# Kernel tuning notes

Hardware: AMD Instinct MI355X
Metric: run time of the kernel (lower is better)

Reference implementation:

```python
import jax, jax.numpy as jnp
import numpy as np

N_NODES = 100000
N_EDGES = 6400000
DIM_FEAT = 5


def setup_inputs() -> dict:
    key = jax.random.key(0)
    k1, k2, k3 = jax.random.split(key, 3)
    features = jax.random.normal(k1, (N_NODES, DIM_FEAT), dtype=jnp.float32)
    src = jax.random.randint(k2, (N_EDGES,), 0, N_NODES, dtype=jnp.int64)
    dst = jax.random.randint(k3, (N_EDGES,), 0, N_NODES, dtype=jnp.int64)
    return {"features": features, "src": src, "dst": dst}


def reference(features, src, dst):
    # copy_u('h','m') then sum('m','h'):
    # h_out[v] = sum over edges (u->v) of features[u]
    msgs = features[src]  # [E, F] gather
    h = jax.ops.segment_sum(msgs, dst, num_segments=N_NODES)  # [N, F]
    return h
```

## Files before the change

kernel.cpp:

```cpp
#include <hip/hip_runtime.h>
#include <hip/hip_bf16.h>


#define NN     100000
#define FD     5
#define NOUTT  (NN * FD)
#define NPS    32
#define NPS_SH 5
#define NB     3125
#define NSB    512
#define BLK    256

typedef int vint4 __attribute__((ext_vector_type(4)));

__device__ inline unsigned bf16rtn(float x) {
    unsigned u = __float_as_uint(x);
    u += 0x7fffu + ((u >> 16) & 1u);
    return u >> 16;
}
__device__ inline float lo16(unsigned v) { return __uint_as_float(v << 16); }
__device__ inline float hi16(unsigned v) { return __uint_as_float(v & 0xffff0000u); }

__global__ __launch_bounds__(BLK) void k2_hist(const int* __restrict__ dst,
                                               unsigned short* __restrict__ bh,
                                               int chunk) {
    __shared__ int h[NB];
    for (int b = threadIdx.x; b < NB; b += BLK) h[b] = 0;
    __syncthreads();
    long long e0 = (long long)blockIdx.x * chunk;
    const vint4* d4 = (const vint4*)(dst + e0);
    int n4 = chunk >> 2;
    int i = threadIdx.x;
    for (; i + 3 * BLK < n4; i += 4 * BLK) {
        vint4 d0 = __builtin_nontemporal_load(&d4[i]);
        vint4 d1 = __builtin_nontemporal_load(&d4[i + BLK]);
        vint4 d2 = __builtin_nontemporal_load(&d4[i + 2 * BLK]);
        vint4 d3 = __builtin_nontemporal_load(&d4[i + 3 * BLK]);
        __builtin_amdgcn_sched_barrier(0);
        atomicAdd(&h[d0[0] >> NPS_SH], 1); atomicAdd(&h[d0[1] >> NPS_SH], 1);
        atomicAdd(&h[d0[2] >> NPS_SH], 1); atomicAdd(&h[d0[3] >> NPS_SH], 1);
        atomicAdd(&h[d1[0] >> NPS_SH], 1); atomicAdd(&h[d1[1] >> NPS_SH], 1);
        atomicAdd(&h[d1[2] >> NPS_SH], 1); atomicAdd(&h[d1[3] >> NPS_SH], 1);
        atomicAdd(&h[d2[0] >> NPS_SH], 1); atomicAdd(&h[d2[1] >> NPS_SH], 1);
        atomicAdd(&h[d2[2] >> NPS_SH], 1); atomicAdd(&h[d2[3] >> NPS_SH], 1);
        atomicAdd(&h[d3[0] >> NPS_SH], 1); atomicAdd(&h[d3[1] >> NPS_SH], 1);
        atomicAdd(&h[d3[2] >> NPS_SH], 1); atomicAdd(&h[d3[3] >> NPS_SH], 1);
    }
    for (; i < n4; i += BLK) {
        vint4 d = __builtin_nontemporal_load(&d4[i]);
        atomicAdd(&h[d[0] >> NPS_SH], 1); atomicAdd(&h[d[1] >> NPS_SH], 1);
        atomicAdd(&h[d[2] >> NPS_SH], 1); atomicAdd(&h[d[3] >> NPS_SH], 1);
    }
    __syncthreads();
    unsigned short* row = bh + (size_t)blockIdx.x * NB;
    for (int b = threadIdx.x; b < NB; b += BLK) row[b] = (unsigned short)h[b];
}

__global__ __launch_bounds__(BLK) void k3_scanblk(unsigned short* __restrict__ bh,
                                                  int* __restrict__ btot) {
    __shared__ int s[BLK];
    int b = blockIdx.x, t = threadIdx.x;
    int v0 = bh[(size_t)(2 * t)     * NB + b];
    int v1 = bh[(size_t)(2 * t + 1) * NB + b];
    int pair = v0 + v1;
    s[t] = pair;
    __syncthreads();
    for (int off = 1; off < BLK; off <<= 1) {
        int v = (t >= off) ? s[t - off] : 0;
        __syncthreads();
        s[t] += v;
        __syncthreads();
    }
    int base = s[t] - pair;
    bh[(size_t)(2 * t)     * NB + b] = (unsigned short)base;
    bh[(size_t)(2 * t + 1) * NB + b] = (unsigned short)(base + v0);
    if (t == BLK - 1) btot[b] = s[t];
}

#define VPT 13
__global__ __launch_bounds__(BLK) void k4_scanbkt(const int* __restrict__ btot,
                                                  int* __restrict__ bbase) {
    __shared__ int s[BLK];
    int t = threadIdx.x;
    int v[VPT], sum = 0;
#pragma unroll
    for (int k = 0; k < VPT; ++k) {
        int i = VPT * t + k;
        v[k] = (i < NB) ? btot[i] : 0;
        sum += v[k];
    }
    s[t] = sum;
    __syncthreads();
    for (int off = 1; off < BLK; off <<= 1) {
        int u = (t >= off) ? s[t - off] : 0;
        __syncthreads();
        s[t] += u;
        __syncthreads();
    }
    int run = s[t] - sum;
#pragma unroll
    for (int k = 0; k < VPT; ++k) {
        int i = VPT * t + k;
        if (i < NB) bbase[i] = run;
        run += v[k];
    }
}

__global__ __launch_bounds__(BLK) void k5_scatter(const int* __restrict__ src,
                                                  const int* __restrict__ dst,
                                                  const unsigned short* __restrict__ bh,
                                                  const int* __restrict__ bbase,
                                                  int* __restrict__ bdata, int chunk) {
    __shared__ int cur[NB];
    int blk = blockIdx.x;
    const unsigned short* row = bh + (size_t)blk * NB;
    for (int b = threadIdx.x; b < NB; b += BLK)
        cur[b] = bbase[b] + (int)row[b];
    __syncthreads();
    long long e0 = (long long)blk * chunk;
    const vint4* d4 = (const vint4*)(dst + e0);
    const vint4* s4 = (const vint4*)(src + e0);
    int n4 = chunk >> 2;
    int i = threadIdx.x;
    for (; i + 3 * BLK < n4; i += 4 * BLK) {
        vint4 d[4], s[4];
#pragma unroll
        for (int k = 0; k < 4; ++k) {
            d[k] = __builtin_nontemporal_load(&d4[i + k * BLK]);
            s[k] = __builtin_nontemporal_load(&s4[i + k * BLK]);
        }
        __builtin_amdgcn_sched_barrier(0);
#pragma unroll
        for (int k = 0; k < 4; ++k) {
#pragma unroll
            for (int j = 0; j < 4; ++j) {
                int vv = d[k][j];
                int uu = s[k][j];
                int b = vv >> NPS_SH;
                int off = atomicAdd(&cur[b], 1);
                bdata[off] = (uu << NPS_SH) | (vv & (NPS - 1));
            }
        }
    }
    for (; i < n4; i += BLK) {
        vint4 d = __builtin_nontemporal_load(&d4[i]);
        vint4 s = __builtin_nontemporal_load(&s4[i]);
#pragma unroll
        for (int j = 0; j < 4; ++j) {
            int vv = d[j];
            int uu = s[j];
            int b = vv >> NPS_SH;
            int off = atomicAdd(&cur[b], 1);
            bdata[off] = (uu << NPS_SH) | (vv & (NPS - 1));
        }
    }
}

__global__ __launch_bounds__(BLK) void k1_pad(const float* __restrict__ f,
                                              uint4* __restrict__ fp) {
    int i = blockIdx.x * BLK + threadIdx.x;
    if (i < NN) {
        const float* r = f + (long long)i * FD;
        unsigned w0 = bf16rtn(r[0]), w1 = bf16rtn(r[1]), w2 = bf16rtn(r[2]);
        unsigned w3 = bf16rtn(r[3]), w4 = bf16rtn(r[4]);
        uint4 o;
        o.x = w0 | (w1 << 16);
        o.y = w2 | (w3 << 16);
        o.z = w4;
        o.w = 0u;
        fp[i] = o;
    }
}

#define UNR 8
__global__ __launch_bounds__(BLK) void k6_gather(const int* __restrict__ bdata,
                                                 const uint4* __restrict__ fp,
                                                 const int* __restrict__ bbase,
                                                 const int* __restrict__ btot,
                                                 float* __restrict__ out) {
    __shared__ float acc[NPS * FD];
    int t = threadIdx.x;
    if (t < NPS * FD) acc[t] = 0.f;
    __syncthreads();
    int b = blockIdx.x;
    int base = bbase[b];
    int n = btot[b];

    int i = t;
    for (; i + (UNR - 1) * BLK < n; i += UNR * BLK) {
        int   l[UNR];
        uint4 g[UNR];
#pragma unroll
        for (int k = 0; k < UNR; ++k) {
            int w = bdata[base + i + k * BLK];
            l[k] = w & (NPS - 1);
            g[k] = fp[w >> NPS_SH];
        }
        __builtin_amdgcn_sched_barrier(0);
#pragma unroll
        for (int k = 0; k < UNR; ++k) {
            float* p = acc + l[k] * FD;
            atomicAdd(&p[0], lo16(g[k].x));
            atomicAdd(&p[1], hi16(g[k].x));
            atomicAdd(&p[2], lo16(g[k].y));
            atomicAdd(&p[3], hi16(g[k].y));
            atomicAdd(&p[4], lo16(g[k].z));
        }
    }
    for (; i < n; i += BLK) {
        int w = bdata[base + i];
        int l = w & (NPS - 1);
        uint4 g = fp[w >> NPS_SH];
        float* p = acc + l * FD;
        atomicAdd(&p[0], lo16(g.x)); atomicAdd(&p[1], hi16(g.x));
        atomicAdd(&p[2], lo16(g.y)); atomicAdd(&p[3], hi16(g.y));
        atomicAdd(&p[4], lo16(g.z));
    }
    __syncthreads();
    if (t < NPS * FD) out[(size_t)b * NPS * FD + t] = acc[t];
}

__global__ void scatter_add_fallback(const float* __restrict__ features,
                                     const int* __restrict__ src,
                                     const int* __restrict__ dst,
                                     float* __restrict__ out, int n_edges) {
    int idx = blockIdx.x * blockDim.x + threadIdx.x;
    int stride = gridDim.x * blockDim.x;
    for (int e = idx; e < n_edges; e += stride) {
        int u = src[e], v = dst[e];
        const float* f = features + (long long)u * FD;
        float* o = out + (long long)v * FD;
#pragma unroll
        for (int k = 0; k < FD; ++k) atomicAdd(&o[k], f[k]);
    }
}

extern "C" void kernel_launch(void* const* d_in, const int* in_sizes, int n_in,
                              void* d_out, int out_size, void* d_ws, size_t ws_size,
                              hipStream_t stream) {
    const float* features = (const float*)d_in[0];
    const int*   src      = (const int*)d_in[1];
    const int*   dst      = (const int*)d_in[2];
    float* out = (float*)d_out;
    int n_edges = in_sizes[1];

    size_t o_bd = 0;
    size_t o_bh = o_bd + (size_t)n_edges * 4;
    size_t o_fp = o_bh;
    size_t sz_overlap = (size_t)NSB * NB * 2;
    size_t sz_fp = (size_t)NN * sizeof(uint4);
    if (sz_fp > sz_overlap) sz_overlap = sz_fp;
    size_t o_bb = o_bh + ((sz_overlap + 15) & ~(size_t)15);
    size_t o_bt = o_bb + (size_t)NB * 4;
    size_t need = o_bt + (size_t)NB * 4;

    bool fast = (out_size == NOUTT) && (in_sizes[0] == NOUTT) &&
                (n_edges % (NSB * 4) == 0) && (need <= ws_size);

    if (fast) {
        char* w = (char*)d_ws;
        int*            bdata = (int*)(w + o_bd);
        unsigned short* bhist = (unsigned short*)(w + o_bh);
        uint4*          fpad  = (uint4*)(w + o_fp);
        int*            bbase = (int*)(w + o_bb);
        int*            btot  = (int*)(w + o_bt);
        int chunk = n_edges / NSB;
        k2_hist  <<<NSB, BLK, 0, stream>>>(dst, bhist, chunk);
        k3_scanblk<<<NB, BLK, 0, stream>>>(bhist, btot);
        k4_scanbkt<<<1,  BLK, 0, stream>>>(btot, bbase);
        k5_scatter<<<NSB, BLK, 0, stream>>>(src, dst, bhist, bbase, bdata, chunk);
        k1_pad   <<<(NN + BLK - 1) / BLK, BLK, 0, stream>>>(features, fpad);
        k6_gather <<<NB, BLK, 0, stream>>>(bdata, fpad, bbase, btot, out);
    } else {
        (void)hipMemsetAsync(d_out, 0, (size_t)out_size * sizeof(float), stream);
        int grid = (n_edges + BLK - 1) / BLK;
        if (grid > 65535) grid = 65535;
        scatter_add_fallback<<<grid, BLK, 0, stream>>>(features, src, dst, out, n_edges);
    }
}
```

Baseline: 379.9 us.

## Stage bucket edge list in LDS and prefetch packed features into cache

The gather kernel now loads each bucket's edge words into shared memory with aligned vector nontemporal loads before the accumulate loop, instead of reading them from global memory inside the loop. The first 256 blocks also touch slices of the padded feature table so it is warm in cache before the random gathers start. Buckets larger than the LDS capacity fall back to global reads for the remainder. Workspace offsets gain padding so the aligned vector over-read stays in bounds. This costs extra LDS, which may lower occupancy, and the warm-up loop adds redundant traffic.

Result: no change. 385.2 us (+1.4%).

```diff
diff --git a/kernel.cpp b/kernel.cpp
--- a/kernel.cpp
+++ b/kernel.cpp
@@ -10,6 +10,7 @@
 #define NB     3125
 #define NSB    512
 #define BLK    256
+#define ECAP   3072
 
 typedef int vint4 __attribute__((ext_vector_type(4)));
 
@@ -178,21 +179,47 @@
                                                  const int* __restrict__ bbase,
                                                  const int* __restrict__ btot,
                                                  float* __restrict__ out) {
+    __shared__ int   ebuf[ECAP];
     __shared__ float acc[NPS * FD];
     int t = threadIdx.x;
     if (t < NPS * FD) acc[t] = 0.f;
-    __syncthreads();
     int b = blockIdx.x;
     int base = bbase[b];
     int n = btot[b];
+    int ns = n < ECAP ? n : ECAP;
+
+    int a0   = base & ~3;
+    int lead = base - a0;
+    int tot4 = (lead + ns + 3) >> 2;
+    const vint4* bd4 = (const vint4*)(bdata + a0);
+    for (int j = t; j < tot4; j += BLK) {
+        vint4 v = __builtin_nontemporal_load(&bd4[j]);
+        int o = j * 4 - lead;
+#pragma unroll
+        for (int q = 0; q < 4; ++q) {
+            int idx = o + q;
+            if (idx >= 0 && idx < ns) ebuf[idx] = v[q];
+        }
+    }
+
+    if (b < 256) {
+        int s0 = (b >> 3) * (NN / 32);
+        unsigned sink = 0;
+        for (int j = t; j < NN / 32; j += BLK) {
+            uint4 v = fp[s0 + j];
+            sink ^= v.x ^ v.y ^ v.z;
+        }
+        asm volatile("" :: "v"(sink));
+    }
+    __syncthreads();
 
     int i = t;
-    for (; i + (UNR - 1) * BLK < n; i += UNR * BLK) {
+    for (; i + (UNR - 1) * BLK < ns; i += UNR * BLK) {
         int   l[UNR];
         uint4 g[UNR];
 #pragma unroll
         for (int k = 0; k < UNR; ++k) {
-            int w = bdata[base + i + k * BLK];
+            int w = ebuf[i + k * BLK];
             l[k] = w & (NPS - 1);
             g[k] = fp[w >> NPS_SH];
         }
@@ -207,7 +234,16 @@
             atomicAdd(&p[4], lo16(g[k].z));
         }
     }
-    for (; i < n; i += BLK) {
+    for (; i < ns; i += BLK) {
+        int w = ebuf[i];
+        int l = w & (NPS - 1);
+        uint4 g = fp[w >> NPS_SH];
+        float* p = acc + l * FD;
+        atomicAdd(&p[0], lo16(g.x)); atomicAdd(&p[1], hi16(g.x));
+        atomicAdd(&p[2], lo16(g.y)); atomicAdd(&p[3], hi16(g.y));
+        atomicAdd(&p[4], lo16(g.z));
+    }
+    for (i = ECAP + t; i < n; i += BLK) {
         int w = bdata[base + i];
         int l = w & (NPS - 1);
         uint4 g = fp[w >> NPS_SH];
@@ -245,7 +281,7 @@
     int n_edges = in_sizes[1];
 
     size_t o_bd = 0;
-    size_t o_bh = o_bd + (size_t)n_edges * 4;
+    size_t o_bh = o_bd + (size_t)n_edges * 4 + 32;
     size_t o_fp = o_bh;
     size_t sz_overlap = (size_t)NSB * NB * 2;
     size_t sz_fp = (size_t)NN * sizeof(uint4);
```

## Split edges into two halves and overlap bucketing stages across halves

Applied to the files above, without the earlier changes.

The edge list is split into two halves with 400 blocks per half. The histogram of the second half now runs in the same launch as the bucket scatter of the first half. The gather of the first half runs together with the scatter of the second half, and a final gather accumulates the second half into the output. The single-block offset scan is fused with the bf16 feature padding, and the gather unroll drops from 8 to 4. This aims to fill idle CUs and hide tail effects between dependent stages, at the cost of more launches, an extra read-modify-write of the output, and 12.5KB of shared memory reserved per block in the fused gather launch, which may lower occupancy.

After: 382.3 us. Within noise of the previous version (+0.6%).

```diff
diff --git a/kernel.cpp b/kernel.cpp
--- a/kernel.cpp
+++ b/kernel.cpp
@@ -8,26 +8,26 @@
 #define NPS    32
 #define NPS_SH 5
 #define NB     3125
-#define NSB    512
+#define NSBH   400
 #define BLK    256
 
 typedef int vint4 __attribute__((ext_vector_type(4)));
 
-__device__ inline unsigned bf16rtn(float x) {
+__device__ __forceinline__ unsigned bf16rtn(float x) {
     unsigned u = __float_as_uint(x);
     u += 0x7fffu + ((u >> 16) & 1u);
     return u >> 16;
 }
-__device__ inline float lo16(unsigned v) { return __uint_as_float(v << 16); }
-__device__ inline float hi16(unsigned v) { return __uint_as_float(v & 0xffff0000u); }
-
-__global__ __launch_bounds__(BLK) void k2_hist(const int* __restrict__ dst,
-                                               unsigned short* __restrict__ bh,
-                                               int chunk) {
-    __shared__ int h[NB];
+__device__ __forceinline__ float lo16(unsigned v) { return __uint_as_float(v << 16); }
+__device__ __forceinline__ float hi16(unsigned v) { return __uint_as_float(v & 0xffff0000u); }
+
+
+__device__ __forceinline__ void k2_body(int bid, const int* __restrict__ dst,
+                                        unsigned short* __restrict__ bh,
+                                        int chunk, int* h) {
     for (int b = threadIdx.x; b < NB; b += BLK) h[b] = 0;
     __syncthreads();
-    long long e0 = (long long)blockIdx.x * chunk;
+    long long e0 = (long long)bid * chunk;
     const vint4* d4 = (const vint4*)(dst + e0);
     int n4 = chunk >> 2;
     int i = threadIdx.x;
@@ -52,72 +52,21 @@
         atomicAdd(&h[d[2] >> NPS_SH], 1); atomicAdd(&h[d[3] >> NPS_SH], 1);
     }
     __syncthreads();
-    unsigned short* row = bh + (size_t)blockIdx.x * NB;
+    unsigned short* row = bh + (size_t)bid * NB;
     for (int b = threadIdx.x; b < NB; b += BLK) row[b] = (unsigned short)h[b];
 }
 
-__global__ __launch_bounds__(BLK) void k3_scanblk(unsigned short* __restrict__ bh,
-                                                  int* __restrict__ btot) {
-    __shared__ int s[BLK];
-    int b = blockIdx.x, t = threadIdx.x;
-    int v0 = bh[(size_t)(2 * t)     * NB + b];
-    int v1 = bh[(size_t)(2 * t + 1) * NB + b];
-    int pair = v0 + v1;
-    s[t] = pair;
-    __syncthreads();
-    for (int off = 1; off < BLK; off <<= 1) {
-        int v = (t >= off) ? s[t - off] : 0;
-        __syncthreads();
-        s[t] += v;
-        __syncthreads();
-    }
-    int base = s[t] - pair;
-    bh[(size_t)(2 * t)     * NB + b] = (unsigned short)base;
-    bh[(size_t)(2 * t + 1) * NB + b] = (unsigned short)(base + v0);
-    if (t == BLK - 1) btot[b] = s[t];
-}
-
-#define VPT 13
-__global__ __launch_bounds__(BLK) void k4_scanbkt(const int* __restrict__ btot,
-                                                  int* __restrict__ bbase) {
-    __shared__ int s[BLK];
-    int t = threadIdx.x;
-    int v[VPT], sum = 0;
-#pragma unroll
-    for (int k = 0; k < VPT; ++k) {
-        int i = VPT * t + k;
-        v[k] = (i < NB) ? btot[i] : 0;
-        sum += v[k];
-    }
-    s[t] = sum;
-    __syncthreads();
-    for (int off = 1; off < BLK; off <<= 1) {
-        int u = (t >= off) ? s[t - off] : 0;
-        __syncthreads();
-        s[t] += u;
-        __syncthreads();
-    }
-    int run = s[t] - sum;
-#pragma unroll
-    for (int k = 0; k < VPT; ++k) {
-        int i = VPT * t + k;
-        if (i < NB) bbase[i] = run;
-        run += v[k];
-    }
-}
-
-__global__ __launch_bounds__(BLK) void k5_scatter(const int* __restrict__ src,
-                                                  const int* __restrict__ dst,
-                                                  const unsigned short* __restrict__ bh,
-                                                  const int* __restrict__ bbase,
-                                                  int* __restrict__ bdata, int chunk) {
-    __shared__ int cur[NB];
-    int blk = blockIdx.x;
-    const unsigned short* row = bh + (size_t)blk * NB;
+__device__ __forceinline__ void k5_body(int bid, const int* __restrict__ src,
+                                        const int* __restrict__ dst,
+                                        const unsigned short* __restrict__ bh,
+                                        const int* __restrict__ bbase,
+                                        int* __restrict__ bdata, int chunk,
+                                        int* cur) {
+    const unsigned short* row = bh + (size_t)bid * NB;
     for (int b = threadIdx.x; b < NB; b += BLK)
         cur[b] = bbase[b] + (int)row[b];
     __syncthreads();
-    long long e0 = (long long)blk * chunk;
+    long long e0 = (long long)bid * chunk;
     const vint4* d4 = (const vint4*)(dst + e0);
     const vint4* s4 = (const vint4*)(src + e0);
     int n4 = chunk >> 2;
@@ -156,36 +105,18 @@
     }
 }
 
-__global__ __launch_bounds__(BLK) void k1_pad(const float* __restrict__ f,
-                                              uint4* __restrict__ fp) {
-    int i = blockIdx.x * BLK + threadIdx.x;
-    if (i < NN) {
-        const float* r = f + (long long)i * FD;
-        unsigned w0 = bf16rtn(r[0]), w1 = bf16rtn(r[1]), w2 = bf16rtn(r[2]);
-        unsigned w3 = bf16rtn(r[3]), w4 = bf16rtn(r[4]);
-        uint4 o;
-        o.x = w0 | (w1 << 16);
-        o.y = w2 | (w3 << 16);
-        o.z = w4;
-        o.w = 0u;
-        fp[i] = o;
-    }
-}
-
-#define UNR 8
-__global__ __launch_bounds__(BLK) void k6_gather(const int* __restrict__ bdata,
-                                                 const uint4* __restrict__ fp,
-                                                 const int* __restrict__ bbase,
-                                                 const int* __restrict__ btot,
-                                                 float* __restrict__ out) {
-    __shared__ float acc[NPS * FD];
+#define UNR 4
+__device__ __forceinline__ void k6_body(int b, const int* __restrict__ bdata,
+                                        const uint4* __restrict__ fp,
+                                        const int* __restrict__ bbase,
+                                        const int* __restrict__ btot,
+                                        float* __restrict__ out, bool addm,
+                                        float* acc) {
     int t = threadIdx.x;
     if (t < NPS * FD) acc[t] = 0.f;
     __syncthreads();
-    int b = blockIdx.x;
     int base = bbase[b];
     int n = btot[b];
-
     int i = t;
     for (; i + (UNR - 1) * BLK < n; i += UNR * BLK) {
         int   l[UNR];
@@ -217,7 +148,138 @@
         atomicAdd(&p[4], lo16(g.z));
     }
     __syncthreads();
-    if (t < NPS * FD) out[(size_t)b * NPS * FD + t] = acc[t];
+    if (t < NPS * FD) {
+        size_t o = (size_t)b * NPS * FD + t;
+        if (addm) out[o] += acc[t];
+        else      out[o] = acc[t];
+    }
+}
+
+__device__ __forceinline__ void k4_body(const int* __restrict__ btot,
+                                        int* __restrict__ bbase, int* s) {
+#define VPT 13
+    int t = threadIdx.x;
+    int v[VPT], sum = 0;
+#pragma unroll
+    for (int k = 0; k < VPT; ++k) {
+        int i = VPT * t + k;
+        v[k] = (i < NB) ? btot[i] : 0;
+        sum += v[k];
+    }
+    s[t] = sum;
+    __syncthreads();
+    for (int off = 1; off < BLK; off <<= 1) {
+        int u = (t >= off) ? s[t - off] : 0;
+        __syncthreads();
+        s[t] += u;
+        __syncthreads();
+    }
+    int run = s[t] - sum;
+#pragma unroll
+    for (int k = 0; k < VPT; ++k) {
+        int i = VPT * t + k;
+        if (i < NB) bbase[i] = run;
+        run += v[k];
+    }
+}
+
+
+__global__ __launch_bounds__(BLK) void g_k2(const int* __restrict__ dst,
+                                            unsigned short* __restrict__ bh,
+                                            int chunk) {
+    __shared__ int h[NB];
+    k2_body(blockIdx.x, dst, bh, chunk, h);
+}
+
+__global__ __launch_bounds__(BLK) void g_k3(unsigned short* __restrict__ bh,
+                                            int* __restrict__ btot) {
+    __shared__ int s[BLK];
+    int b = blockIdx.x, t = threadIdx.x;
+    int r0 = 2 * t, r1 = 2 * t + 1;
+    int v0 = (r0 < NSBH) ? (int)bh[(size_t)r0 * NB + b] : 0;
+    int v1 = (r1 < NSBH) ? (int)bh[(size_t)r1 * NB + b] : 0;
+    int pair = v0 + v1;
+    s[t] = pair;
+    __syncthreads();
+    for (int off = 1; off < BLK; off <<= 1) {
+        int v = (t >= off) ? s[t - off] : 0;
+        __syncthreads();
+        s[t] += v;
+        __syncthreads();
+    }
+    int base = s[t] - pair;
+    if (r0 < NSBH) bh[(size_t)r0 * NB + b] = (unsigned short)base;
+    if (r1 < NSBH) bh[(size_t)r1 * NB + b] = (unsigned short)(base + v0);
+    if (t == BLK - 1) btot[b] = s[t];
+}
+
+__global__ __launch_bounds__(BLK) void g_k4(const int* __restrict__ btot,
+                                            int* __restrict__ bbase) {
+    __shared__ int s[BLK];
+    k4_body(btot, bbase, s);
+}
+
+__global__ __launch_bounds__(BLK) void g_k4k1(const int* __restrict__ btot,
+                                              int* __restrict__ bbase,
+                                              const float* __restrict__ f,
+                                              uint4* __restrict__ fp) {
+    __shared__ int s[BLK];
+    if (blockIdx.x == 0) {
+        k4_body(btot, bbase, s);
+    } else {
+        int i = (blockIdx.x - 1) * BLK + threadIdx.x;
+        if (i < NN) {
+            const float* r = f + (long long)i * FD;
+            unsigned w0 = bf16rtn(r[0]), w1 = bf16rtn(r[1]), w2 = bf16rtn(r[2]);
+            unsigned w3 = bf16rtn(r[3]), w4 = bf16rtn(r[4]);
+            uint4 o;
+            o.x = w0 | (w1 << 16);
+            o.y = w2 | (w3 << 16);
+            o.z = w4;
+            o.w = 0u;
+            fp[i] = o;
+        }
+    }
+}
+
+__global__ __launch_bounds__(BLK) void g_k5k2(const int* __restrict__ src,
+                                              const int* __restrict__ dst,
+                                              const unsigned short* __restrict__ bhA,
+                                              const int* __restrict__ bbaseA,
+                                              int* __restrict__ bdata,
+                                              unsigned short* __restrict__ bhB,
+                                              int chunk, int half) {
+    __shared__ int u[NB];
+    int bid = blockIdx.x;
+    if (bid < NSBH) k5_body(bid, src, dst, bhA, bbaseA, bdata, chunk, u);
+    else            k2_body(bid - NSBH, dst + half, bhB, chunk, u);
+}
+
+__global__ __launch_bounds__(BLK) void g_k6k5(const int* __restrict__ src,
+                                              const int* __restrict__ dst,
+                                              const unsigned short* __restrict__ bhB,
+                                              const int* __restrict__ bbaseB,
+                                              int* __restrict__ bdata,
+                                              const uint4* __restrict__ fp,
+                                              const int* __restrict__ bbaseA,
+                                              const int* __restrict__ btotA,
+                                              float* __restrict__ out,
+                                              int chunk, int half) {
+    __shared__ int u[NB];
+    int bid = blockIdx.x;
+    if (bid < NSBH)
+        k5_body(bid, src + half, dst + half, bhB, bbaseB, bdata + half, chunk, u);
+    else
+        k6_body(bid - NSBH, bdata, fp, bbaseA, btotA, out, false, (float*)u);
+}
+
+__global__ __launch_bounds__(BLK) void g_k6(const int* __restrict__ bdata,
+                                            const uint4* __restrict__ fp,
+                                            const int* __restrict__ bbaseB,
+                                            const int* __restrict__ btotB,
+                                            float* __restrict__ out, int half) {
+    __shared__ float acc[NPS * FD];
+    k6_body(blockIdx.x, bdata + half, fp, bbaseB, btotB, out, true, acc);
 }
 
 __global__ void scatter_add_fallback(const float* __restrict__ features,
@@ -244,33 +306,46 @@
     float* out = (float*)d_out;
     int n_edges = in_sizes[1];
 
-    size_t o_bd = 0;
-    size_t o_bh = o_bd + (size_t)n_edges * 4;
-    size_t o_fp = o_bh;
-    size_t sz_overlap = (size_t)NSB * NB * 2;
+    size_t o_bd  = 0;
+    size_t o_r1  = o_bd + (size_t)n_edges * 4 + 64;
+    size_t sz_r1 = (size_t)NSBH * NB * 2;
     size_t sz_fp = (size_t)NN * sizeof(uint4);
-    if (sz_fp > sz_overlap) sz_overlap = sz_fp;
-    size_t o_bb = o_bh + ((sz_overlap + 15) & ~(size_t)15);
-    size_t o_bt = o_bb + (size_t)NB * 4;
-    size_t need = o_bt + (size_t)NB * 4;
+    if (sz_fp > sz_r1) sz_r1 = sz_fp;
+    size_t o_bhB = o_r1 + ((sz_r1 + 15) & ~(size_t)15);
+    size_t o_bbA = o_bhB + (((size_t)NSBH * NB * 2 + 15) & ~(size_t)15);
+    size_t o_btA = o_bbA + (size_t)NB * 4;
+    size_t o_bbB = o_btA + (size_t)NB * 4;
+    size_t o_btB = o_bbB + (size_t)NB * 4;
+    size_t need  = o_btB + (size_t)NB * 4;
 
     bool fast = (out_size == NOUTT) && (in_sizes[0] == NOUTT) &&
-                (n_edges % (NSB * 4) == 0) && (need <= ws_size);
+                (n_edges % (2 * NSBH * 4) == 0) && (need <= ws_size);
 
     if (fast) {
         char* w = (char*)d_ws;
         int*            bdata = (int*)(w + o_bd);
-        unsigned short* bhist = (unsigned short*)(w + o_bh);
-        uint4*          fpad  = (uint4*)(w + o_fp);
-        int*            bbase = (int*)(w + o_bb);
-        int*            btot  = (int*)(w + o_bt);
-        int chunk = n_edges / NSB;
-        k2_hist  <<<NSB, BLK, 0, stream>>>(dst, bhist, chunk);
-        k3_scanblk<<<NB, BLK, 0, stream>>>(bhist, btot);
-        k4_scanbkt<<<1,  BLK, 0, stream>>>(btot, bbase);
-        k5_scatter<<<NSB, BLK, 0, stream>>>(src, dst, bhist, bbase, bdata, chunk);
-        k1_pad   <<<(NN + BLK - 1) / BLK, BLK, 0, stream>>>(features, fpad);
-        k6_gather <<<NB, BLK, 0, stream>>>(bdata, fpad, bbase, btot, out);
+        unsigned short* bhA   = (unsigned short*)(w + o_r1);
+        uint4*          fpad  = (uint4*)(w + o_r1);
+        unsigned short* bhB   = (unsigned short*)(w + o_bhB);
+        int*            bbaseA = (int*)(w + o_bbA);
+        int*            btotA  = (int*)(w + o_btA);
+        int*            bbaseB = (int*)(w + o_bbB);
+        int*            btotB  = (int*)(w + o_btB);
+        int half  = n_edges / 2;
+        int chunk = half / NSBH;
+
+        g_k2  <<<NSBH, BLK, 0, stream>>>(dst, bhA, chunk);
+        g_k3  <<<NB,   BLK, 0, stream>>>(bhA, btotA);
+        g_k4  <<<1,    BLK, 0, stream>>>(btotA, bbaseA);
+        g_k5k2<<<2 * NSBH, BLK, 0, stream>>>(src, dst, bhA, bbaseA,
+                                             bdata, bhB, chunk, half);
+        g_k3  <<<NB,   BLK, 0, stream>>>(bhB, btotB);
+        g_k4k1<<<1 + (NN + BLK - 1) / BLK, BLK, 0, stream>>>(btotB, bbaseB,
+                                                             features, fpad);
+        g_k6k5<<<NSBH + NB, BLK, 0, stream>>>(src, dst, bhB, bbaseB, bdata,
+                                              fpad, bbaseA, btotA, out,
+                                              chunk, half);
+        g_k6  <<<NB,   BLK, 0, stream>>>(bdata, fpad, bbaseB, btotB, out, half);
     } else {
         (void)hipMemsetAsync(d_out, 0, (size_t)out_size * sizeof(float), stream);
         int grid = (n_edges + BLK - 1) / BLK;
```

## Two-level source-then-destination bucket sort to localize feature gathers

Applied to the files above, without the earlier changes.

Replaces the single destination-bucket sort with a two-pass scheme. Edges are first bucketed by source range (256 buckets), so feature gathers hit a small cache-resident window. Features are then written with a destination-local index into a 12-byte record array, which a per-destination-bucket kernel reduces in LDS. The histogram, feature packing and hist2 zeroing are fused into one launch. The cost is an extra pass over the edges, a larger 12-byte intermediate array, and single-block serial scans. The old path is kept as a secondary fallback.

After: 382.6 us. No clear change (+0.7%).

```diff
diff --git a/kernel.cpp b/kernel.cpp
--- a/kernel.cpp
+++ b/kernel.cpp
@@ -5,219 +5,436 @@
 #define NN     100000
 #define FD     5
 #define NOUTT  (NN * FD)
-#define NPS    32
-#define NPS_SH 5
-#define NB     3125
-#define NSB    512
 #define BLK    256
 
+#define NSRCB  256
+#define SRCW   391
+#define NDSTB  256
+#define DSTW   391
+#define NCH    400
+#define DSTMSK 0x1FFFF
+
 typedef int vint4 __attribute__((ext_vector_type(4)));
 
-__device__ inline unsigned bf16rtn(float x) {
+__device__ __forceinline__ unsigned bf16rtn(float x) {
     unsigned u = __float_as_uint(x);
     u += 0x7fffu + ((u >> 16) & 1u);
     return u >> 16;
 }
-__device__ inline float lo16(unsigned v) { return __uint_as_float(v << 16); }
-__device__ inline float hi16(unsigned v) { return __uint_as_float(v & 0xffff0000u); }
-
-__global__ __launch_bounds__(BLK) void k2_hist(const int* __restrict__ dst,
-                                               unsigned short* __restrict__ bh,
-                                               int chunk) {
-    __shared__ int h[NB];
-    for (int b = threadIdx.x; b < NB; b += BLK) h[b] = 0;
+__device__ __forceinline__ float lo16(unsigned v) { return __uint_as_float(v << 16); }
+__device__ __forceinline__ float hi16(unsigned v) { return __uint_as_float(v & 0xffff0000u); }
+
+#define NPACKB ((NN + BLK - 1) / BLK)
+#define NZB    64
+__global__ __launch_bounds__(BLK) void n1_hist_pack(const int* __restrict__ src,
+                                                    const float* __restrict__ f,
+                                                    unsigned short* __restrict__ bh1,
+                                                    uint4* __restrict__ fp,
+                                                    int* __restrict__ hist2,
+                                                    int chunk) {
+    int bid = blockIdx.x;
+    if (bid < NCH) {
+        __shared__ int h[NSRCB];
+        if (threadIdx.x < NSRCB) h[threadIdx.x] = 0;
+        __syncthreads();
+        long long e0 = (long long)bid * chunk;
+        const vint4* s4 = (const vint4*)(src + e0);
+        int n4 = chunk >> 2;
+        for (int i = threadIdx.x; i < n4; i += BLK) {
+            vint4 s = __builtin_nontemporal_load(&s4[i]);
+            atomicAdd(&h[s[0] / SRCW], 1); atomicAdd(&h[s[1] / SRCW], 1);
+            atomicAdd(&h[s[2] / SRCW], 1); atomicAdd(&h[s[3] / SRCW], 1);
+        }
+        __syncthreads();
+        if (threadIdx.x < NSRCB)
+            bh1[(size_t)bid * NSRCB + threadIdx.x] = (unsigned short)h[threadIdx.x];
+    } else if (bid < NCH + NPACKB) {
+        int i = (bid - NCH) * BLK + threadIdx.x;
+        if (i < NN) {
+            const float* r = f + (long long)i * FD;
+            uint4 o;
+            o.x = bf16rtn(r[0]) | (bf16rtn(r[1]) << 16);
+            o.y = bf16rtn(r[2]) | (bf16rtn(r[3]) << 16);
+            o.z = bf16rtn(r[4]);
+            o.w = 0u;
+            fp[i] = o;
+        }
+    } else {
+        int base = (bid - NCH - NPACKB) * (NSRCB * NDSTB / NZB);
+        for (int j = threadIdx.x; j < NSRCB * NDSTB / NZB; j += BLK)
+            hist2[base + j] = 0;
+    }
+}
+
+__global__ __launch_bounds__(BLK) void n2_scan1(unsigned short* __restrict__ bh1,
+                                                int* __restrict__ sbtot) {
+    __shared__ int s[BLK];
+    int b = blockIdx.x, t = threadIdx.x;
+    int r0 = 2 * t, r1 = 2 * t + 1;
+    int v0 = (r0 < NCH) ? (int)bh1[(size_t)r0 * NSRCB + b] : 0;
+    int v1 = (r1 < NCH) ? (int)bh1[(size_t)r1 * NSRCB + b] : 0;
+    int pair = v0 + v1;
+    s[t] = pair;
+    __syncthreads();
+    for (int off = 1; off < BLK; off <<= 1) {
+        int v = (t >= off) ? s[t - off] : 0;
+        __syncthreads();
+        s[t] += v;
+        __syncthreads();
+    }
+    int base = s[t] - pair;
+    if (r0 < NCH) bh1[(size_t)r0 * NSRCB + b] = (unsigned short)base;
+    if (r1 < NCH) bh1[(size_t)r1 * NSRCB + b] = (unsigned short)(base + v0);
+    if (t == BLK - 1) sbtot[b] = s[t];
+}
+
+__global__ __launch_bounds__(BLK) void n3_base1(const int* __restrict__ sbtot,
+                                                int* __restrict__ sbbase) {
+    __shared__ int s[BLK];
+    int t = threadIdx.x;
+    int x = sbtot[t];
+    s[t] = x;
+    __syncthreads();
+    for (int off = 1; off < BLK; off <<= 1) {
+        int v = (t >= off) ? s[t - off] : 0;
+        __syncthreads();
+        s[t] += v;
+        __syncthreads();
+    }
+    sbbase[t] = s[t] - x;
+}
+
+__global__ __launch_bounds__(BLK) void n4_scatter1(const int* __restrict__ src,
+                                                   const int* __restrict__ dst,
+                                                   const unsigned short* __restrict__ bh1,
+                                                   const int* __restrict__ sbbase,
+                                                   int* __restrict__ srt1, int chunk) {
+    __shared__ int cur[NSRCB];
+    int bid = blockIdx.x, t = threadIdx.x;
+    if (t < NSRCB) cur[t] = sbbase[t] + (int)bh1[(size_t)bid * NSRCB + t];
+    __syncthreads();
+    long long e0 = (long long)bid * chunk;
+    const vint4* s4 = (const vint4*)(src + e0);
+    const vint4* d4 = (const vint4*)(dst + e0);
+    int n4 = chunk >> 2;
+    int i = t;
+    for (; i + 3 * BLK < n4; i += 4 * BLK) {
+        vint4 sv[4], dv[4];
+#pragma unroll
+        for (int k = 0; k < 4; ++k) {
+            sv[k] = __builtin_nontemporal_load(&s4[i + k * BLK]);
+            dv[k] = __builtin_nontemporal_load(&d4[i + k * BLK]);
+        }
+        __builtin_amdgcn_sched_barrier(0);
+#pragma unroll
+        for (int k = 0; k < 4; ++k) {
+#pragma unroll
+            for (int j = 0; j < 4; ++j) {
+                int u = sv[k][j], v = dv[k][j];
+                int sb = u / SRCW;
+                int off = atomicAdd(&cur[sb], 1);
+                srt1[off] = ((u - sb * SRCW) << 17) | v;
+            }
+        }
+    }
+    for (; i < n4; i += BLK) {
+        vint4 sv = __builtin_nontemporal_load(&s4[i]);
+        vint4 dv = __builtin_nontemporal_load(&d4[i]);
+#pragma unroll
+        for (int j = 0; j < 4; ++j) {
+            int u = sv[j], v = dv[j];
+            int sb = u / SRCW;
+            int off = atomicAdd(&cur[sb], 1);
+            srt1[off] = ((u - sb * SRCW) << 17) | v;
+        }
+    }
+}
+
+__global__ __launch_bounds__(BLK) void n5_hist2(const int* __restrict__ srt1,
+                                                const int* __restrict__ sbbase,
+                                                const int* __restrict__ sbtot,
+                                                int* __restrict__ hist2) {
+    __shared__ int h[NDSTB];
+    int s = blockIdx.x >> 1, half = blockIdx.x & 1, t = threadIdx.x;
+    if (t < NDSTB) h[t] = 0;
+    __syncthreads();
+    int cnt = sbtot[s];
+    int c0 = cnt >> 1;
+    int start = sbbase[s] + (half ? c0 : 0);
+    int num = half ? (cnt - c0) : c0;
+    for (int i = t; i < num; i += BLK) {
+        int w = srt1[start + i];
+        atomicAdd(&h[(w & DSTMSK) / DSTW], 1);
+    }
+    __syncthreads();
+    if (t < NDSTB && h[t] > 0) atomicAdd(&hist2[s * NDSTB + t], h[t]);
+}
+
+__global__ __launch_bounds__(BLK) void n6_base2(const int* __restrict__ hist2,
+                                                int* __restrict__ base2,
+                                                int* __restrict__ dbase,
+                                                int* __restrict__ dcnt) {
+    __shared__ int s[BLK];
+    int d = threadIdx.x;
+    int tot = 0;
+    for (int ss = 0; ss < NSRCB; ++ss) tot += hist2[ss * NDSTB + d];
+    dcnt[d] = tot;
+    s[d] = tot;
+    __syncthreads();
+    for (int off = 1; off < BLK; off <<= 1) {
+        int v = (d >= off) ? s[d - off] : 0;
+        __syncthreads();
+        s[d] += v;
+        __syncthreads();
+    }
+    int run = s[d] - tot;
+    dbase[d] = run;
+    for (int ss = 0; ss < NSRCB; ++ss) {
+        base2[ss * NDSTB + d] = run;
+        run += hist2[ss * NDSTB + d];
+    }
+}
+
+__global__ __launch_bounds__(BLK) void n7_scatter2(const int* __restrict__ srt1,
+                                                   const uint4* __restrict__ fp,
+                                                   const int* __restrict__ sbbase,
+                                                   const int* __restrict__ sbtot,
+                                                   const int* __restrict__ base2,
+                                                   int* __restrict__ srt2) {
+    __shared__ int cur[NDSTB];
+    int s = blockIdx.x, t = threadIdx.x;
+    if (t < NDSTB) cur[t] = base2[s * NDSTB + t];
+    __syncthreads();
+    int base = sbbase[s];
+    int cnt = sbtot[s];
+    int u0 = s * SRCW;
+    int i = t;
+    for (; i + 3 * BLK < cnt; i += 4 * BLK) {
+        int w[4];
+        uint4 g[4];
+#pragma unroll
+        for (int k = 0; k < 4; ++k) w[k] = srt1[base + i + k * BLK];
+#pragma unroll
+        for (int k = 0; k < 4; ++k) g[k] = fp[u0 + ((unsigned)w[k] >> 17)];
+        __builtin_amdgcn_sched_barrier(0);
+#pragma unroll
+        for (int k = 0; k < 4; ++k) {
+            int v = w[k] & DSTMSK;
+            int d = v / DSTW;
+            int dl = v - d * DSTW;
+            int slot = atomicAdd(&cur[d], 1);
+            int* p = srt2 + (size_t)slot * 3;
+            p[0] = (int)g[k].x;
+            p[1] = (int)g[k].y;
+            p[2] = (int)((g[k].z & 0xFFFFu) | ((unsigned)dl << 16));
+        }
+    }
+    for (; i < cnt; i += BLK) {
+        int w = srt1[base + i];
+        uint4 g = fp[u0 + ((unsigned)w >> 17)];
+        int v = w & DSTMSK;
+        int d = v / DSTW;
+        int dl = v - d * DSTW;
+        int slot = atomicAdd(&cur[d], 1);
+        int* p = srt2 + (size_t)slot * 3;
+        p[0] = (int)g.x;
+        p[1] = (int)g.y;
+        p[2] = (int)((g.z & 0xFFFFu) | ((unsigned)dl << 16));
+    }
+}
+
+__global__ __launch_bounds__(BLK) void n8_reduce(const int* __restrict__ srt2,
+                                                 const int* __restrict__ dbase,
+                                                 const int* __restrict__ dcnt,
+                                                 float* __restrict__ out) {
+    __shared__ float acc[DSTW * FD];
+    int d = blockIdx.x, t = threadIdx.x;
+    for (int j = t; j < DSTW * FD; j += BLK) acc[j] = 0.f;
+    __syncthreads();
+    int base = dbase[d];
+    int n = dcnt[d];
+    int i = t;
+    for (; i + 3 * BLK < n; i += 4 * BLK) {
+        int r[4][3];
+#pragma unroll
+        for (int k = 0; k < 4; ++k) {
+            const int* p = srt2 + (size_t)(base + i + k * BLK) * 3;
+            r[k][0] = p[0]; r[k][1] = p[1]; r[k][2] = p[2];
+        }
+        __builtin_amdgcn_sched_barrier(0);
+#pragma unroll
+        for (int k = 0; k < 4; ++k) {
+            int dl = (unsigned)r[k][2] >> 16;
+            float* p = acc + dl * FD;
+            atomicAdd(&p[0], lo16((unsigned)r[k][0]));
+            atomicAdd(&p[1], hi16((unsigned)r[k][0]));
+            atomicAdd(&p[2], lo16((unsigned)r[k][1]));
+            atomicAdd(&p[3], hi16((unsigned)r[k][1]));
+            atomicAdd(&p[4], lo16((unsigned)r[k][2]));
+        }
+    }
+    for (; i < n; i += BLK) {
+        const int* p = srt2 + (size_t)(base + i) * 3;
+        int r0 = p[0], r1 = p[1], r2 = p[2];
+        int dl = (unsigned)r2 >> 16;
+        float* a = acc + dl * FD;
+        atomicAdd(&a[0], lo16((unsigned)r0)); atomicAdd(&a[1], hi16((unsigned)r0));
+        atomicAdd(&a[2], lo16((unsigned)r1)); atomicAdd(&a[3], hi16((unsigned)r1));
+        atomicAdd(&a[4], lo16((unsigned)r2));
+    }
+    __syncthreads();
+    int node0 = d * DSTW;
+    int nn = NN - node0; if (nn > DSTW) nn = DSTW;
+    int nfl = nn * FD;
+    float* o = out + (long long)node0 * FD;
+    for (int j = t; j < nfl; j += BLK) o[j] = acc[j];
+}
+
+#define M_NPS 32
+#define M_SH  5
+#define M_NB  3125
+#define M_NSB 512
+__global__ __launch_bounds__(BLK) void m2_hist(const int* __restrict__ dst,
+                                               unsigned short* __restrict__ bh, int chunk) {
+    __shared__ int h[M_NB];
+    for (int b = threadIdx.x; b < M_NB; b += BLK) h[b] = 0;
     __syncthreads();
     long long e0 = (long long)blockIdx.x * chunk;
     const vint4* d4 = (const vint4*)(dst + e0);
     int n4 = chunk >> 2;
-    int i = threadIdx.x;
-    for (; i + 3 * BLK < n4; i += 4 * BLK) {
-        vint4 d0 = __builtin_nontemporal_load(&d4[i]);
-        vint4 d1 = __builtin_nontemporal_load(&d4[i + BLK]);
-        vint4 d2 = __builtin_nontemporal_load(&d4[i + 2 * BLK]);
-        vint4 d3 = __builtin_nontemporal_load(&d4[i + 3 * BLK]);
-        __builtin_amdgcn_sched_barrier(0);
-        atomicAdd(&h[d0[0] >> NPS_SH], 1); atomicAdd(&h[d0[1] >> NPS_SH], 1);
-        atomicAdd(&h[d0[2] >> NPS_SH], 1); atomicAdd(&h[d0[3] >> NPS_SH], 1);
-        atomicAdd(&h[d1[0] >> NPS_SH], 1); atomicAdd(&h[d1[1] >> NPS_SH], 1);
-        atomicAdd(&h[d1[2] >> NPS_SH], 1); atomicAdd(&h[d1[3] >> NPS_SH], 1);
-        atomicAdd(&h[d2[0] >> NPS_SH], 1); atomicAdd(&h[d2[1] >> NPS_SH], 1);
-        atomicAdd(&h[d2[2] >> NPS_SH], 1); atomicAdd(&h[d2[3] >> NPS_SH], 1);
-        atomicAdd(&h[d3[0] >> NPS_SH], 1); atomicAdd(&h[d3[1] >> NPS_SH], 1);
-        atomicAdd(&h[d3[2] >> NPS_SH], 1); atomicAdd(&h[d3[3] >> NPS_SH], 1);
-    }
-    for (; i < n4; i += BLK) {
+    for (int i = threadIdx.x; i < n4; i += BLK) {
         vint4 d = __builtin_nontemporal_load(&d4[i]);
-        atomicAdd(&h[d[0] >> NPS_SH], 1); atomicAdd(&h[d[1] >> NPS_SH], 1);
-        atomicAdd(&h[d[2] >> NPS_SH], 1); atomicAdd(&h[d[3] >> NPS_SH], 1);
-    }
-    __syncthreads();
-    unsigned short* row = bh + (size_t)blockIdx.x * NB;
-    for (int b = threadIdx.x; b < NB; b += BLK) row[b] = (unsigned short)h[b];
-}
-
-__global__ __launch_bounds__(BLK) void k3_scanblk(unsigned short* __restrict__ bh,
-                                                  int* __restrict__ btot) {
+        atomicAdd(&h[d[0] >> M_SH], 1); atomicAdd(&h[d[1] >> M_SH], 1);
+        atomicAdd(&h[d[2] >> M_SH], 1); atomicAdd(&h[d[3] >> M_SH], 1);
+    }
+    __syncthreads();
+    unsigned short* row = bh + (size_t)blockIdx.x * M_NB;
+    for (int b = threadIdx.x; b < M_NB; b += BLK) row[b] = (unsigned short)h[b];
+}
+__global__ __launch_bounds__(BLK) void m3_scan(unsigned short* __restrict__ bh,
+                                               int* __restrict__ btot) {
     __shared__ int s[BLK];
     int b = blockIdx.x, t = threadIdx.x;
-    int v0 = bh[(size_t)(2 * t)     * NB + b];
-    int v1 = bh[(size_t)(2 * t + 1) * NB + b];
+    int v0 = bh[(size_t)(2 * t) * M_NB + b];
+    int v1 = bh[(size_t)(2 * t + 1) * M_NB + b];
     int pair = v0 + v1;
     s[t] = pair;
     __syncthreads();
     for (int off = 1; off < BLK; off <<= 1) {
         int v = (t >= off) ? s[t - off] : 0;
-        __syncthreads();
-        s[t] += v;
-        __syncthreads();
+        __syncthreads(); s[t] += v; __syncthreads();
     }
     int base = s[t] - pair;
-    bh[(size_t)(2 * t)     * NB + b] = (unsigned short)base;
-    bh[(size_t)(2 * t + 1) * NB + b] = (unsigned short)(base + v0);
+    bh[(size_t)(2 * t) * M_NB + b] = (unsigned short)base;
+    bh[(size_t)(2 * t + 1) * M_NB + b] = (unsigned short)(base + v0);
     if (t == BLK - 1) btot[b] = s[t];
 }
-
-#define VPT 13
-__global__ __launch_bounds__(BLK) void k4_scanbkt(const int* __restrict__ btot,
-                                                  int* __restrict__ bbase) {
+#define M_VPT 13
+__global__ __launch_bounds__(BLK) void m4_base(const int* __restrict__ btot,
+                                               int* __restrict__ bbase) {
     __shared__ int s[BLK];
     int t = threadIdx.x;
-    int v[VPT], sum = 0;
-#pragma unroll
-    for (int k = 0; k < VPT; ++k) {
-        int i = VPT * t + k;
-        v[k] = (i < NB) ? btot[i] : 0;
+    int v[M_VPT], sum = 0;
+#pragma unroll
+    for (int k = 0; k < M_VPT; ++k) {
+        int i = M_VPT * t + k;
+        v[k] = (i < M_NB) ? btot[i] : 0;
         sum += v[k];
     }
     s[t] = sum;
     __syncthreads();
     for (int off = 1; off < BLK; off <<= 1) {
         int u = (t >= off) ? s[t - off] : 0;
-        __syncthreads();
-        s[t] += u;
-        __syncthreads();
+        __syncthreads(); s[t] += u; __syncthreads();
     }
     int run = s[t] - sum;
 #pragma unroll
-    for (int k = 0; k < VPT; ++k) {
-        int i = VPT * t + k;
-        if (i < NB) bbase[i] = run;
+    for (int k = 0; k < M_VPT; ++k) {
+        int i = M_VPT * t + k;
+        if (i < M_NB) bbase[i] = run;
         run += v[k];
     }
 }
-
-__global__ __launch_bounds__(BLK) void k5_scatter(const int* __restrict__ src,
+__global__ __launch_bounds__(BLK) void m5_scatter(const int* __restrict__ src,
                                                   const int* __restrict__ dst,
                                                   const unsigned short* __restrict__ bh,
                                                   const int* __restrict__ bbase,
                                                   int* __restrict__ bdata, int chunk) {
-    __shared__ int cur[NB];
+    __shared__ int cur[M_NB];
     int blk = blockIdx.x;
-    const unsigned short* row = bh + (size_t)blk * NB;
-    for (int b = threadIdx.x; b < NB; b += BLK)
-        cur[b] = bbase[b] + (int)row[b];
+    const unsigned short* row = bh + (size_t)blk * M_NB;
+    for (int b = threadIdx.x; b < M_NB; b += BLK) cur[b] = bbase[b] + (int)row[b];
     __syncthreads();
     long long e0 = (long long)blk * chunk;
     const vint4* d4 = (const vint4*)(dst + e0);
     const vint4* s4 = (const vint4*)(src + e0);
     int n4 = chunk >> 2;
-    int i = threadIdx.x;
-    for (; i + 3 * BLK < n4; i += 4 * BLK) {
-        vint4 d[4], s[4];
-#pragma unroll
-        for (int k = 0; k < 4; ++k) {
-            d[k] = __builtin_nontemporal_load(&d4[i + k * BLK]);
-            s[k] = __builtin_nontemporal_load(&s4[i + k * BLK]);
-        }
-        __builtin_amdgcn_sched_barrier(0);
-#pragma unroll
-        for (int k = 0; k < 4; ++k) {
-#pragma unroll
-            for (int j = 0; j < 4; ++j) {
-                int vv = d[k][j];
-                int uu = s[k][j];
-                int b = vv >> NPS_SH;
-                int off = atomicAdd(&cur[b], 1);
-                bdata[off] = (uu << NPS_SH) | (vv & (NPS - 1));
-            }
-        }
-    }
-    for (; i < n4; i += BLK) {
+    for (int i = threadIdx.x; i < n4; i += BLK) {
         vint4 d = __builtin_nontemporal_load(&d4[i]);
         vint4 s = __builtin_nontemporal_load(&s4[i]);
 #pragma unroll
         for (int j = 0; j < 4; ++j) {
-            int vv = d[j];
-            int uu = s[j];
-            int b = vv >> NPS_SH;
+            int vv = d[j], uu = s[j];
+            int b = vv >> M_SH;
             int off = atomicAdd(&cur[b], 1);
-            bdata[off] = (uu << NPS_SH) | (vv & (NPS - 1));
-        }
-    }
-}
-
-__global__ __launch_bounds__(BLK) void k1_pad(const float* __restrict__ f,
+            bdata[off] = (uu << M_SH) | (vv & (M_NPS - 1));
+        }
+    }
+}
+__global__ __launch_bounds__(BLK) void m1_pad(const float* __restrict__ f,
                                               uint4* __restrict__ fp) {
     int i = blockIdx.x * BLK + threadIdx.x;
     if (i < NN) {
         const float* r = f + (long long)i * FD;
-        unsigned w0 = bf16rtn(r[0]), w1 = bf16rtn(r[1]), w2 = bf16rtn(r[2]);
-        unsigned w3 = bf16rtn(r[3]), w4 = bf16rtn(r[4]);
         uint4 o;
-        o.x = w0 | (w1 << 16);
-        o.y = w2 | (w3 << 16);
-        o.z = w4;
+        o.x = bf16rtn(r[0]) | (bf16rtn(r[1]) << 16);
+        o.y = bf16rtn(r[2]) | (bf16rtn(r[3]) << 16);
+        o.z = bf16rtn(r[4]);
         o.w = 0u;
         fp[i] = o;
     }
 }
-
-#define UNR 8
-__global__ __launch_bounds__(BLK) void k6_gather(const int* __restrict__ bdata,
+__global__ __launch_bounds__(BLK) void m6_gather(const int* __restrict__ bdata,
                                                  const uint4* __restrict__ fp,
                                                  const int* __restrict__ bbase,
                                                  const int* __restrict__ btot,
                                                  float* __restrict__ out) {
-    __shared__ float acc[NPS * FD];
+    __shared__ float acc[M_NPS * FD];
     int t = threadIdx.x;
-    if (t < NPS * FD) acc[t] = 0.f;
+    if (t < M_NPS * FD) acc[t] = 0.f;
     __syncthreads();
     int b = blockIdx.x;
     int base = bbase[b];
     int n = btot[b];
-
     int i = t;
-    for (; i + (UNR - 1) * BLK < n; i += UNR * BLK) {
-        int   l[UNR];
-        uint4 g[UNR];
-#pragma unroll
-        for (int k = 0; k < UNR; ++k) {
+    for (; i + 3 * BLK < n; i += 4 * BLK) {
+        int l[4]; uint4 g[4];
+#pragma unroll
+        for (int k = 0; k < 4; ++k) {
             int w = bdata[base + i + k * BLK];
-            l[k] = w & (NPS - 1);
-            g[k] = fp[w >> NPS_SH];
+            l[k] = w & (M_NPS - 1);
+            g[k] = fp[w >> M_SH];
         }
         __builtin_amdgcn_sched_barrier(0);
 #pragma unroll
-        for (int k = 0; k < UNR; ++k) {
+        for (int k = 0; k < 4; ++k) {
             float* p = acc + l[k] * FD;
-            atomicAdd(&p[0], lo16(g[k].x));
-            atomicAdd(&p[1], hi16(g[k].x));
-            atomicAdd(&p[2], lo16(g[k].y));
-            atomicAdd(&p[3], hi16(g[k].y));
+            atomicAdd(&p[0], lo16(g[k].x)); atomicAdd(&p[1], hi16(g[k].x));
+            atomicAdd(&p[2], lo16(g[k].y)); atomicAdd(&p[3], hi16(g[k].y));
             atomicAdd(&p[4], lo16(g[k].z));
         }
     }
     for (; i < n; i += BLK) {
         int w = bdata[base + i];
-        int l = w & (NPS - 1);
-        uint4 g = fp[w >> NPS_SH];
+        int l = w & (M_NPS - 1);
+        uint4 g = fp[w >> M_SH];
         float* p = acc + l * FD;
         atomicAdd(&p[0], lo16(g.x)); atomicAdd(&p[1], hi16(g.x));
         atomicAdd(&p[2], lo16(g.y)); atomicAdd(&p[3], hi16(g.y));
         atomicAdd(&p[4], lo16(g.z));
     }
     __syncthreads();
-    if (t < NPS * FD) out[(size_t)b * NPS * FD + t] = acc[t];
+    if (t < M_NPS * FD) out[(size_t)b * M_NPS * FD + t] = acc[t];
 }
 
 __global__ void scatter_add_fallback(const float* __restrict__ features,
@@ -235,6 +452,8 @@
     }
 }
 
+static inline size_t al16(size_t x) { return (x + 15) & ~(size_t)15; }
+
 extern "C" void kernel_launch(void* const* d_in, const int* in_sizes, int n_in,
                               void* d_out, int out_size, void* d_ws, size_t ws_size,
                               hipStream_t stream) {
@@ -243,38 +462,75 @@
     const int*   dst      = (const int*)d_in[2];
     float* out = (float*)d_out;
     int n_edges = in_sizes[1];
-
-    size_t o_bd = 0;
-    size_t o_bh = o_bd + (size_t)n_edges * 4;
-    size_t o_fp = o_bh;
-    size_t sz_overlap = (size_t)NSB * NB * 2;
-    size_t sz_fp = (size_t)NN * sizeof(uint4);
-    if (sz_fp > sz_overlap) sz_overlap = sz_fp;
-    size_t o_bb = o_bh + ((sz_overlap + 15) & ~(size_t)15);
-    size_t o_bt = o_bb + (size_t)NB * 4;
-    size_t need = o_bt + (size_t)NB * 4;
-
-    bool fast = (out_size == NOUTT) && (in_sizes[0] == NOUTT) &&
-                (n_edges % (NSB * 4) == 0) && (need <= ws_size);
-
-    if (fast) {
-        char* w = (char*)d_ws;
-        int*            bdata = (int*)(w + o_bd);
-        unsigned short* bhist = (unsigned short*)(w + o_bh);
+    char* w = (char*)d_ws;
+
+    size_t o_s1 = 0;
+    size_t o_s2 = al16(o_s1 + (size_t)n_edges * 4);
+    size_t o_fp = al16(o_s2 + (size_t)n_edges * 12);
+    size_t o_b1 = al16(o_fp + (size_t)NN * 16);
+    size_t o_st = al16(o_b1 + (size_t)NCH * NSRCB * 2);
+    size_t o_sb = al16(o_st + NSRCB * 4);
+    size_t o_h2 = al16(o_sb + NSRCB * 4);
+    size_t o_b2 = al16(o_h2 + (size_t)NSRCB * NDSTB * 4);
+    size_t o_db = al16(o_b2 + (size_t)NSRCB * NDSTB * 4);
+    size_t o_dc = al16(o_db + NDSTB * 4);
+    size_t needN = o_dc + NDSTB * 4;
+
+    bool okN = (out_size == NOUTT) && (in_sizes[0] == NOUTT) &&
+               (n_edges % (NCH * 4) == 0) && (needN <= ws_size);
+
+    if (okN) {
+        int*            srt1  = (int*)(w + o_s1);
+        int*            srt2  = (int*)(w + o_s2);
         uint4*          fpad  = (uint4*)(w + o_fp);
-        int*            bbase = (int*)(w + o_bb);
-        int*            btot  = (int*)(w + o_bt);
-        int chunk = n_edges / NSB;
-        k2_hist  <<<NSB, BLK, 0, stream>>>(dst, bhist, chunk);
-        k3_scanblk<<<NB, BLK, 0, stream>>>(bhist, btot);
-        k4_scanbkt<<<1,  BLK, 0, stream>>>(btot, bbase);
-        k5_scatter<<<NSB, BLK, 0, stream>>>(src, dst, bhist, bbase, bdata, chunk);
-        k1_pad   <<<(NN + BLK - 1) / BLK, BLK, 0, stream>>>(features, fpad);
-        k6_gather <<<NB, BLK, 0, stream>>>(bdata, fpad, bbase, btot, out);
-    } else {
-        (void)hipMemsetAsync(d_out, 0, (size_t)out_size * sizeof(float), stream);
-        int grid = (n_edges + BLK - 1) / BLK;
-        if (grid > 65535) grid = 65535;
-        scatter_add_fallback<<<grid, BLK, 0, stream>>>(features, src, dst, out, n_edges);
-    }
-}
+        unsigned short* bh1   = (unsigned short*)(w + o_b1);
+        int*            sbtot = (int*)(w + o_st);
+        int*            sbbase= (int*)(w + o_sb);
+        int*            hist2 = (int*)(w + o_h2);
+        int*            base2 = (int*)(w + o_b2);
+        int*            dbase = (int*)(w + o_db);
+        int*            dcnt  = (int*)(w + o_dc);
+        int chunk = n_edges / NCH;
+        n1_hist_pack<<<NCH + NPACKB + NZB, BLK, 0, stream>>>(src, features, bh1,
+                                                             fpad, hist2, chunk);
+        n2_scan1   <<<NSRCB, BLK, 0, stream>>>(bh1, sbtot);
+        n3_base1   <<<1, BLK, 0, stream>>>(sbtot, sbbase);
+        n4_scatter1<<<NCH, BLK, 0, stream>>>(src, dst, bh1, sbbase, srt1, chunk);
+        n5_hist2   <<<2 * NSRCB, BLK, 0, stream>>>(srt1, sbbase, sbtot, hist2);
+        n6_base2   <<<1, BLK, 0, stream>>>(hist2, base2, dbase, dcnt);
+        n7_scatter2<<<NSRCB, BLK, 0, stream>>>(srt1, fpad, sbbase, sbtot, base2, srt2);
+        n8_reduce  <<<NDSTB, BLK, 0, stream>>>(srt2, dbase, dcnt, out);
+        return;
+    }
+
+    size_t mo_bd = 0;
+    size_t mo_r1 = al16(mo_bd + (size_t)n_edges * 4 + 32);
+    size_t sz_r1 = (size_t)M_NSB * M_NB * 2;
+    size_t sz_fp = (size_t)NN * 16;
+    if (sz_fp > sz_r1) sz_r1 = sz_fp;
+    size_t mo_bb = al16(mo_r1 + sz_r1);
+    size_t mo_bt = mo_bb + (size_t)M_NB * 4;
+    size_t needM = mo_bt + (size_t)M_NB * 4;
+    bool okM = (out_size == NOUTT) && (in_sizes[0] == NOUTT) &&
+               (n_edges % (M_NSB * 4) == 0) && (needM <= ws_size);
+    if (okM) {
+        int*            bdata = (int*)(w + mo_bd);
+        unsigned short* bhist = (unsigned short*)(w + mo_r1);
+        uint4*          fpad  = (uint4*)(w + mo_r1);
+        int*            bbase = (int*)(w + mo_bb);
+        int*            btot  = (int*)(w + mo_bt);
+        int chunk = n_edges / M_NSB;
+        m2_hist   <<<M_NSB, BLK, 0, stream>>>(dst, bhist, chunk);
+        m3_scan   <<<M_NB, BLK, 0, stream>>>(bhist, btot);
+        m4_base   <<<1, BLK, 0, stream>>>(btot, bbase);
+        m5_scatter<<<M_NSB, BLK, 0, stream>>>(src, dst, bhist, bbase, bdata, chunk);
+        m1_pad    <<<(NN + BLK - 1) / BLK, BLK, 0, stream>>>(features, fpad);
+        m6_gather <<<M_NB, BLK, 0, stream>>>(bdata, fpad, bbase, btot, out);
+        return;
+    }
+
+    (void)hipMemsetAsync(d_out, 0, (size_t)out_size * sizeof(float), stream);
+    int grid = (n_edges + BLK - 1) / BLK;
+    if (grid > 65535) grid = 65535;
+    scatter_add_fallback<<<grid, BLK, 0, stream>>>(features, src, dst, out, n_edges);
+}
```
